# Kernel tuning notes

Hardware: AMD Instinct MI355X
Metric: run time of the kernel (lower is better)

The kernel has to match this reference:

```python
import jax, jax.numpy as jnp
import numpy as np

V, D, H, N, L = 400000, 300, 300, 346, 50


def _lstm_scan(x, Wih, Whh, b, reverse):
    # x: (L, N, din); torch gate order i, f, g, o
    Hh = Whh.shape[1]
    def step(carry, xt):
        h, c = carry
        g = xt @ Wih.T + h @ Whh.T + b
        i, f, gg, o = jnp.split(g, 4, axis=-1)
        c = jax.nn.sigmoid(f) * c + jax.nn.sigmoid(i) * jnp.tanh(gg)
        h = jax.nn.sigmoid(o) * jnp.tanh(c)
        return (h, c), h
    h0 = jnp.zeros((x.shape[1], Hh), x.dtype)
    (hT, _), outs = jax.lax.scan(step, (h0, h0), x, reverse=reverse)
    return hT, outs  # outs stacked in original time order


def _gate(h, W, U):
    # Faithful to torch gate_module: g_i broadcast over rows makes
    # g.repeat @ h_x == g_i * sum(h_x) and (1-g).repeat @ h_c_rep == (1-g_i)*m*h_c
    h_c = h[0]
    h_x = h[1:]
    m = h_x.shape[0]
    g = jax.nn.sigmoid(h_x @ W + h_c @ U)  # (m, 1)
    h_tuta = g * jnp.sum(h_x, axis=0) + (1.0 - g) * (m * h_c)
    return jnp.concatenate([h_c[None, :], h_tuta], axis=0)


def _gat(h, mask, W, a):
    # standard pyGAT GraphAttentionLayer (concat=True -> elu), alpha=0.01
    Wh = h @ W                              # (N, out)
    F = W.shape[1]
    e = jax.nn.leaky_relu((Wh @ a[:F]) + (Wh @ a[F:]).T, 0.01)  # (N, N)
    att = jax.nn.softmax(jnp.where(mask, e, -9e15), axis=1)
    return jax.nn.elu(att @ Wh)


def _forward(emb, Wih_l0f, Whh_l0f, b_l0f, Wih_l0b, Whh_l0b, b_l0b,
             Wih_l1f, Whh_l1f, b_l1f, Wih_l1b, Whh_l1b, b_l1b,
             W_gat, a_gat, gate_W, gate_U, FC1, FC2, Wlin, blin,
             tokens, adj):
    tok = tokens[0]                        # (N, L)
    x = jnp.swapaxes(emb[tok], 0, 1)       # (L, N, 300)
    hf0, of0 = _lstm_scan(x, Wih_l0f, Whh_l0f, b_l0f, False)
    hb0, ob0 = _lstm_scan(x, Wih_l0b, Whh_l0b, b_l0b, True)
    o0 = jnp.concatenate([of0, ob0], axis=-1)   # (L, N, 600)
    hf1, _ = _lstm_scan(o0, Wih_l1f, Whh_l1f, b_l1f, False)
    hb1, _ = _lstm_scan(o0, Wih_l1b, Whh_l1b, b_l1b, True)
    # h_n layout [l0f, l0b, l1f, l1b] -> per-node concat = 1200
    hs0 = jnp.concatenate([hf0, hb0, hf1, hb1], axis=-1)
    mask = adj > 0
    hs1 = _gat(jnp.concatenate([hs0, _gate(hs0, gate_W, gate_U)], axis=1), mask, W_gat, a_gat)
    hs2 = _gat(jnp.concatenate([hs1, _gate(hs1, gate_W, gate_U)], axis=1), mask, W_gat, a_gat)
    hc = jnp.broadcast_to(hs2[0], hs2.shape)          # repeat(346, 1)
    hc3 = jnp.tanh(jnp.concatenate([hc, hs2, hc * hs2, hc - hs2], axis=1) @ FC1)
    b_att = jnp.tanh(hc3 @ FC2)                       # (N, 1)
    ea = jnp.concatenate([jnp.mean(hs2, axis=0, keepdims=True), b_att.T @ hs2], axis=1)
    return jax.nn.softmax(ea @ Wlin.T + blin, axis=1)  # (1, 2)


def setup_inputs() -> dict:
    key = jax.random.key(0)
    ks = iter(jax.random.split(key, 40))
    def rn(shape, scale=0.05):
        return jax.random.normal(next(ks), shape, dtype=jnp.float32) * scale
    inp = {}
    inp["tokens"] = jax.random.randint(next(ks), (1, N, L), 0, V)
    inp["adj"] = jax.random.randint(next(ks), (N, N), 0, 2).astype(jnp.int32)
    inp["emb"] = rn((V, D), 1.0)
    for name, din in (("l0f", D), ("l0b", D), ("l1f", 2 * H), ("l1b", 2 * H)):
        inp[f"Wih_{name}"] = rn((4 * H, din))
        inp[f"Whh_{name}"] = rn((4 * H, H))
        inp[f"b_{name}"] = rn((4 * H,))
    inp["W_gat"] = rn((2400, 1200))
    inp["a_gat"] = rn((2400, 1))
    inp["gate_W"] = rn((1200, 1))
    inp["gate_U"] = rn((1200, 1))
    inp["FC1"] = rn((4800, 9600), 0.01)
    inp["FC2"] = rn((9600, 1), 0.01)
    inp["Wlin"] = rn((2, 2400))
    inp["blin"] = rn((2,))
    return inp


def reference(tokens, adj, emb, Wih_l0f, Whh_l0f, b_l0f, Wih_l0b, Whh_l0b, b_l0b,
              Wih_l1f, Whh_l1f, b_l1f, Wih_l1b, Whh_l1b, b_l1b,
              W_gat, a_gat, gate_W, gate_U, FC1, FC2, Wlin, blin):
    return _forward(emb, Wih_l0f, Whh_l0f, b_l0f, Wih_l0b, Whh_l0b, b_l0b,
                    Wih_l1f, Whh_l1f, b_l1f, Wih_l1b, Whh_l1b, b_l1b,
                    W_gat, a_gat, gate_W, gate_U, FC1, FC2, Wlin, blin,
                    tokens, adj)
```

## Files before the change

### kernel.cpp

```cpp
#include <hip/hip_runtime.h>
#include <hip/hip_bf16.h>
#include <math.h>

typedef __hip_bfloat16 bf16;
typedef __attribute__((ext_vector_type(8))) short bf16x8;
typedef __attribute__((ext_vector_type(4))) short bf16x4;
typedef __attribute__((ext_vector_type(4))) float f32x4;

constexpr int kN  = 346;
constexpr int kL  = 50;
constexpr int kD  = 300;
constexpr int kH  = 300;
constexpr int kG  = 1200;
constexpr int kNL = kN * kL;
constexpr int kNLp = 17408;
constexpr int kNp  = 384;
constexpr int kKp0 = 320;
constexpr int kKp1 = 608;
constexpr int kGp  = 1280;
constexpr int kHB  = 384;

__device__ inline float toF(float v) { return v; }
__device__ inline float toF(bf16 v) { return __bfloat162float(v); }
__device__ inline void storeC(float* p, float v) { *p = v; }
__device__ inline void storeC(bf16* p, float v) { *p = __float2bfloat16(v); }
__device__ inline float sigf(float x) { return 1.f / (1.f + expf(-x)); }
__device__ inline float bfbits2f(unsigned short u) {
    unsigned int x = ((unsigned int)u) << 16;
    float f; __builtin_memcpy(&f, &x, 4); return f;
}
__device__ inline short f2bf_bits(float f) {
    bf16 b = __float2bfloat16(f);
    short s; __builtin_memcpy(&s, &b, 2); return s;
}

template <int EPI, typename CT>
__global__ __launch_bounds__(256) void gemm_mfma(
    const bf16* __restrict__ A, const bf16* __restrict__ B, CT* __restrict__ C,
    int M, int N, int K, int lda, int ldb, int ldc,
    long sAz, long sBz, long sCz,
    const bf16* __restrict__ P, long sPz, const float* __restrict__ bias, long sbz)
{
    const short* Ag = (const short*)A + (size_t)blockIdx.z * sAz;
    const short* Bg = (const short*)B + (size_t)blockIdx.z * sBz;
    CT* Cg = C + (size_t)blockIdx.z * sCz;
    (void)P; (void)sPz; (void)bias; (void)sbz;

    __shared__ short As[128 * 40];
    __shared__ short Bs[128 * 40];
    int tid = threadIdx.x;
    int row0 = blockIdx.y * 128, col0 = blockIdx.x * 128;
    int wave = tid >> 6, lane = tid & 63;
    int wr = (wave >> 1) * 64, wc = (wave & 1) * 64;
    int lrow = lane & 15, lq = lane >> 4;

    f32x4 acc[4][4];
#pragma unroll
    for (int i = 0; i < 4; ++i)
#pragma unroll
        for (int j = 0; j < 4; ++j) acc[i][j] = (f32x4){0.f, 0.f, 0.f, 0.f};

    int sr = tid >> 2;
    int sc = (tid & 3) * 8;
    for (int k0 = 0; k0 < K; k0 += 32) {
        *(bf16x8*)&As[sr * 40 + sc]        = *(const bf16x8*)&Ag[(size_t)(row0 + sr) * lda + k0 + sc];
        *(bf16x8*)&As[(sr + 64) * 40 + sc] = *(const bf16x8*)&Ag[(size_t)(row0 + sr + 64) * lda + k0 + sc];
        *(bf16x8*)&Bs[sr * 40 + sc]        = *(const bf16x8*)&Bg[(size_t)(col0 + sr) * ldb + k0 + sc];
        *(bf16x8*)&Bs[(sr + 64) * 40 + sc] = *(const bf16x8*)&Bg[(size_t)(col0 + sr + 64) * ldb + k0 + sc];
        __syncthreads();
        bf16x8 aF[4], bF[4];
#pragma unroll
        for (int i = 0; i < 4; ++i) aF[i] = *(const bf16x8*)&As[(wr + i * 16 + lrow) * 40 + lq * 8];
#pragma unroll
        for (int j = 0; j < 4; ++j) bF[j] = *(const bf16x8*)&Bs[(wc + j * 16 + lrow) * 40 + lq * 8];
#pragma unroll
        for (int i = 0; i < 4; ++i)
#pragma unroll
            for (int j = 0; j < 4; ++j)
                acc[i][j] = __builtin_amdgcn_mfma_f32_16x16x32_bf16(aF[i], bF[j], acc[i][j], 0, 0, 0);
        __syncthreads();
    }
#pragma unroll
    for (int i = 0; i < 4; ++i) {
#pragma unroll
        for (int r = 0; r < 4; ++r) {
            int gm = row0 + wr + i * 16 + lq * 4 + r;
            if (gm >= M) continue;
#pragma unroll
            for (int j = 0; j < 4; ++j) {
                int gn = col0 + wc + j * 16 + lrow;
                if (gn >= N) continue;
                float v = acc[i][j][r];
                if constexpr (EPI == 3) v = v > 0.f ? v : (expf(v) - 1.f);
                if constexpr (EPI == 4) v = tanhf(v);
                storeC(&Cg[(size_t)gm * ldc + gn], v);
            }
        }
    }
}

__global__ void transpose_conv(const float* __restrict__ in, bf16* __restrict__ out,
                               int R, int Cc, int Rpad, int Cpad) {
    __shared__ float tile[32][33];
    int bc = blockIdx.x * 32, br = blockIdx.y * 32;
    int tx = threadIdx.x & 31, ty = threadIdx.x >> 5;
#pragma unroll
    for (int k = 0; k < 4; ++k) {
        int r = br + ty + 8 * k, c = bc + tx;
        tile[ty + 8 * k][tx] = (r < R && c < Cc) ? in[(size_t)r * Cc + c] : 0.f;
    }
    __syncthreads();
#pragma unroll
    for (int k = 0; k < 4; ++k) {
        int c = bc + ty + 8 * k, r = br + tx;
        if (c < Cpad && r < Rpad) out[(size_t)c * Rpad + r] = __float2bfloat16(tile[tx][ty + 8 * k]);
    }
}

__global__ void convert_pad_perm(const float* __restrict__ in, bf16* __restrict__ out,
                                 int Cc, int Cpad) {
    int idx = blockIdx.x * 256 + threadIdx.x;
    if (idx >= kGp * Cpad) return;
    int rp = idx / Cpad, c = idx - rp * Cpad;
    int j = rp >> 2, q = rp & 3;
    float v = (j < kH && c < Cc) ? in[(size_t)(q * kH + j) * Cc + c] : 0.f;
    out[idx] = __float2bfloat16(v);
}

__global__ void pack_biases_perm(const float* b0f, const float* b0b, const float* b1f,
                                 const float* b1b, float* b0, float* b1) {
    int i = blockIdx.x * 256 + threadIdx.x;
    if (i >= 2 * kGp) return;
    int dir = i / kGp, rp = i - dir * kGp;
    int j = rp >> 2, q = rp & 3;
    float v0 = 0.f, v1 = 0.f;
    if (j < kH) {
        v0 = dir ? b0b[q * kH + j] : b0f[q * kH + j];
        v1 = dir ? b1b[q * kH + j] : b1f[q * kH + j];
    }
    b0[i] = v0; b1[i] = v1;
}

__global__ void gather_kernel(const int* __restrict__ tokens, const float* __restrict__ emb,
                              bf16* __restrict__ x) {
    int idx = blockIdx.x * 256 + threadIdx.x;
    if (idx >= kNLp * kKp0) return;
    int row = idx / kKp0, d = idx - row * kKp0;
    float v = 0.f;
    if (row < kNL && d < kD) {
        int l = row / kN, n = row - l * kN;
        v = emb[(size_t)tokens[n * kL + l] * kD + d];
    }
    x[idx] = __float2bfloat16(v);
}

__device__ inline void group_barrier(int* bar, int target) {
    __syncthreads();
    if (threadIdx.x == 0) {
        __threadfence();
        __hip_atomic_fetch_add(bar, 1, __ATOMIC_RELAXED, __HIP_MEMORY_SCOPE_AGENT);
        while (__hip_atomic_load(bar, __ATOMIC_RELAXED, __HIP_MEMORY_SCOPE_AGENT) < target)
            __builtin_amdgcn_s_sleep(2);
    }
    __syncthreads();
    __threadfence();
}

template <bool WRITE_O0>
__global__ __launch_bounds__(256, 1) void lstm_scan_fused(
    const bf16* __restrict__ WhhP,
    const bf16* __restrict__ P,
    const float* __restrict__ biasP,
    bf16* __restrict__ hst,
    bf16* __restrict__ o0,
    int* __restrict__ bars)
{
    __shared__ short Bs[10][128][32];
    __shared__ float Gs[4 * 32 * 128];

    const int tid = threadIdx.x;
    const int bx  = blockIdx.x;
    const int cb  = bx % 10;
    const int rb  = (bx / 10) % 3;
    const int dir = bx / 30;
    int* bar = bars + dir * 3 + rb;

    const int wave = tid >> 6, lane = tid & 63;
    const int wr = (wave >> 1) * 64, wc = (wave & 1) * 64;
    const int lrow = lane & 15, lq = lane >> 4;
    const int col0 = cb * 128, row0 = rb * 128;

    {
        const short* Bg = (const short*)WhhP + (size_t)dir * kGp * kKp0;
        int sr = tid >> 2;
        int g  = tid & 3;
#pragma unroll
        for (int ch = 0; ch < 10; ++ch) {
            *(bf16x8*)&Bs[ch][sr][(g ^ ((sr >> 1) & 3)) * 8] =
                *(const bf16x8*)&Bg[(size_t)(col0 + sr) * kKp0 + ch * 32 + g * 8];
            *(bf16x8*)&Bs[ch][sr + 64][(g ^ (((sr + 64) >> 1) & 3)) * 8] =
                *(const bf16x8*)&Bg[(size_t)(col0 + sr + 64) * kKp0 + ch * 32 + g * 8];
        }
    }

    const int jj0 = (tid >> 5) * 4;
    const int pr0 = (tid & 31) * 4;
    const int jg0 = cb * 32 + jj0;
    const bool jok = jg0 < kH;

    float bias[4][4];
#pragma unroll
    for (int m = 0; m < 4; ++m) {
        f32x4 b4 = *(const f32x4*)&biasP[dir * kGp + col0 + (jj0 + m) * 4];
#pragma unroll
        for (int q = 0; q < 4; ++q) bias[m][q] = b4[q];
    }
    float cst[4][4];
#pragma unroll
    for (int m = 0; m < 4; ++m)
#pragma unroll
        for (int r = 0; r < 4; ++r) cst[m][r] = 0.f;

    short* o0s = (short*)o0;
    __syncthreads();

#pragma unroll 1
    for (int t = 0; t < kL; ++t) {
        const short* hr = (const short*)hst + ((size_t)(t & 1) * 2 + dir) * (kHB * kKp0);
        short* hw = (short*)hst + ((size_t)((t + 1) & 1) * 2 + dir) * (kHB * kKp0);
        const int teff = dir ? (kL - 1 - t) : t;
        const short* Pt = (const short*)P + (size_t)dir * kNL * kG + (size_t)teff * kN * kG;

        bf16x4 pv[4][4];
        if (jok) {
#pragma unroll
            for (int m = 0; m < 4; ++m)
#pragma unroll
                for (int rr = 0; rr < 4; ++rr) {
                    int rg = row0 + pr0 + rr;
                    if (rg < kN)
                        pv[m][rr] = *(const bf16x4*)&Pt[(size_t)rg * kG + (size_t)(jg0 + m) * 4];
                }
        }

        f32x4 acc[4][4];
#pragma unroll
        for (int i = 0; i < 4; ++i)
#pragma unroll
            for (int j = 0; j < 4; ++j) acc[i][j] = (f32x4){0.f, 0.f, 0.f, 0.f};

#pragma unroll
        for (int ch = 0; ch < 10; ++ch) {
            bf16x8 aF[4], bF[4];
#pragma unroll
            for (int i = 0; i < 4; ++i)
                aF[i] = *(const bf16x8*)&hr[(size_t)(row0 + wr + i * 16 + lrow) * kKp0 + ch * 32 + lq * 8];
#pragma unroll
            for (int j = 0; j < 4; ++j) {
                int brow = wc + j * 16 + lrow;
                bF[j] = *(const bf16x8*)&Bs[ch][brow][(lq ^ ((brow >> 1) & 3)) * 8];
            }
#pragma unroll
            for (int i = 0; i < 4; ++i)
#pragma unroll
                for (int j = 0; j < 4; ++j)
                    acc[i][j] = __builtin_amdgcn_mfma_f32_16x16x32_bf16(aF[i], bF[j], acc[i][j], 0, 0, 0);
        }

#pragma unroll
        for (int i = 0; i < 4; ++i) {
            int r0 = wr + i * 16 + lq * 4;
#pragma unroll
            for (int j = 0; j < 4; ++j) {
                int c = wc + j * 16 + lrow;
                int q = c & 3, jj = c >> 2;
                *(f32x4*)&Gs[(q * 32 + jj) * 128 + (r0 ^ ((jj & 7) << 2))] = acc[i][j];
            }
        }
        __syncthreads();

        if (jok) {
            float hval[4][4];
#pragma unroll
            for (int m = 0; m < 4; ++m) {
                int jjl = jj0 + m;
                int sw = (jjl & 7) << 2;
                f32x4 gi4 = *(const f32x4*)&Gs[(0 * 32 + jjl) * 128 + (pr0 ^ sw)];
                f32x4 gf4 = *(const f32x4*)&Gs[(1 * 32 + jjl) * 128 + (pr0 ^ sw)];
                f32x4 gg4 = *(const f32x4*)&Gs[(2 * 32 + jjl) * 128 + (pr0 ^ sw)];
                f32x4 go4 = *(const f32x4*)&Gs[(3 * 32 + jjl) * 128 + (pr0 ^ sw)];
#pragma unroll
                for (int rr = 0; rr < 4; ++rr) {
                    int rg = row0 + pr0 + rr;
                    if (rg >= kN) continue;
                    float iv = sigf(gi4[rr] + bfbits2f((unsigned short)pv[m][rr][0]) + bias[m][0]);
                    float fv = sigf(gf4[rr] + bfbits2f((unsigned short)pv[m][rr][1]) + bias[m][1]);
                    float gv = tanhf(gg4[rr] + bfbits2f((unsigned short)pv[m][rr][2]) + bias[m][2]);
                    float ov = sigf(go4[rr] + bfbits2f((unsigned short)pv[m][rr][3]) + bias[m][3]);
                    float cc = fv * cst[m][rr] + iv * gv;
                    cst[m][rr] = cc;
                    hval[rr][m] = ov * tanhf(cc);
                }
            }
#pragma unroll
            for (int rr = 0; rr < 4; ++rr) {
                int rg = row0 + pr0 + rr;
                if (rg >= kN) continue;
                bf16x4 hv;
#pragma unroll
                for (int m = 0; m < 4; ++m) hv[m] = f2bf_bits(hval[rr][m]);
                *(bf16x4*)&hw[(size_t)rg * kKp0 + jg0] = hv;
                if constexpr (WRITE_O0)
                    *(bf16x4*)&o0s[((size_t)teff * kN + rg) * kKp1 + dir * kH + jg0] = hv;
            }
        }

        group_barrier(bar, 10 * (t + 1));
    }
}

__global__ void concat_hs0(const bf16* __restrict__ hbf0, const bf16* __restrict__ hbf1,
                           float* __restrict__ hs0) {
    int idx = blockIdx.x * 256 + threadIdx.x;
    if (idx >= kN * kG) return;
    int r = idx / kG, c = idx - r * kG;
    float v;
    if (c < 300)       v = toF(hbf0[(size_t)r * kKp0 + c]);
    else if (c < 600)  v = toF(hbf0[(size_t)(kNp + r) * kKp0 + (c - 300)]);
    else if (c < 900)  v = toF(hbf1[(size_t)r * kKp0 + (c - 600)]);
    else               v = toF(hbf1[(size_t)(kNp + r) * kKp0 + (c - 900)]);
    hs0[idx] = v;
}

__global__ void colsum_kernel(const float* __restrict__ hs, float* __restrict__ sum_hx) {
    int c = blockIdx.x * 256 + threadIdx.x;
    if (c >= kG) return;
    float s = 0.f;
    for (int r = 1; r < kN; ++r) s += hs[(size_t)r * kG + c];
    sum_hx[c] = s;
}

__global__ void gate_rows(const float* __restrict__ hs, const float* __restrict__ gW,
                          const float* __restrict__ gU, const float* __restrict__ sum_hx,
                          bf16* __restrict__ hin) {
    __shared__ float red[256];
    int n = blockIdx.x, tid = threadIdx.x;
    for (int c = tid; c < kG; c += 256)
        hin[(size_t)n * 2400 + c] = __float2bfloat16(hs[(size_t)n * kG + c]);
    if (n == 0) {
        for (int c = tid; c < kG; c += 256)
            hin[1200 + c] = __float2bfloat16(hs[c]);
        return;
    }
    float dw = 0.f, du = 0.f;
    for (int c = tid; c < kG; c += 256) {
        dw += hs[(size_t)n * kG + c] * gW[c];
        du += hs[c] * gU[c];
    }
    red[tid] = dw; __syncthreads();
    for (int s = 128; s > 0; s >>= 1) { if (tid < s) red[tid] += red[tid + s]; __syncthreads(); }
    float sdw = red[0]; __syncthreads();
    red[tid] = du; __syncthreads();
    for (int s = 128; s > 0; s >>= 1) { if (tid < s) red[tid] += red[tid + s]; __syncthreads(); }
    float sdu = red[0]; __syncthreads();
    float gval = sigf(sdw + sdu);
    for (int c = tid; c < kG; c += 256) {
        float v = gval * sum_hx[c] + (1.f - gval) * (345.f * hs[c]);
        hin[(size_t)n * 2400 + 1200 + c] = __float2bfloat16(v);
    }
}

__global__ void gat_scores(const float* __restrict__ Wh, const float* __restrict__ a,
                           float* __restrict__ s1, float* __restrict__ s2) {
    __shared__ float red[256];
    int n = blockIdx.x, tid = threadIdx.x;
    float d1 = 0.f, d2 = 0.f;
    for (int c = tid; c < kG; c += 256) {
        float w = Wh[(size_t)n * kG + c];
        d1 += w * a[c];
        d2 += w * a[kG + c];
    }
    red[tid] = d1; __syncthreads();
    for (int s = 128; s > 0; s >>= 1) { if (tid < s) red[tid] += red[tid + s]; __syncthreads(); }
    if (tid == 0) s1[n] = red[0];
    __syncthreads();
    red[tid] = d2; __syncthreads();
    for (int s = 128; s > 0; s >>= 1) { if (tid < s) red[tid] += red[tid + s]; __syncthreads(); }
    if (tid == 0) s2[n] = red[0];
}

__global__ void gat_softmax(const float* __restrict__ s1, const float* __restrict__ s2,
                            const int* __restrict__ adj, bf16* __restrict__ att) {
    __shared__ float red[256];
    __shared__ float sh_m, sh_s;
    int i = blockIdx.x, tid = threadIdx.x;
    float s1i = s1[i];
    float m = -1e30f;
    for (int j = tid; j < kN; j += 256) {
        if (adj[i * kN + j] > 0) {
            float e = s1i + s2[j];
            e = e > 0.f ? e : 0.01f * e;
            m = fmaxf(m, e);
        }
    }
    red[tid] = m; __syncthreads();
    for (int s = 128; s > 0; s >>= 1) { if (tid < s) red[tid] = fmaxf(red[tid], red[tid + s]); __syncthreads(); }
    if (tid == 0) sh_m = red[0];
    __syncthreads();
    m = sh_m;
    float sum = 0.f;
    for (int j = tid; j < kN; j += 256) {
        if (adj[i * kN + j] > 0) {
            float e = s1i + s2[j];
            e = e > 0.f ? e : 0.01f * e;
            sum += expf(e - m);
        }
    }
    red[tid] = sum; __syncthreads();
    for (int s = 128; s > 0; s >>= 1) { if (tid < s) red[tid] += red[tid + s]; __syncthreads(); }
    if (tid == 0) sh_s = red[0];
    __syncthreads();
    float inv = sh_s > 0.f ? 1.f / sh_s : 0.f;
    for (int j = tid; j < kN; j += 256) {
        float v = 0.f;
        if (adj[i * kN + j] > 0) {
            float e = s1i + s2[j];
            e = e > 0.f ? e : 0.01f * e;
            v = expf(e - m) * inv;
        }
        att[(size_t)i * 352 + j] = __float2bfloat16(v);
    }
}

__global__ void build_cat4(const float* __restrict__ hs2, bf16* __restrict__ cat4) {
    int idx = blockIdx.x * 256 + threadIdx.x;
    if (idx >= kN * 4800) return;
    int r = idx / 4800, c = idx - r * 4800;
    int chunk = c / kG, cc = c - chunk * kG;
    float hc = hs2[cc];
    float hv = hs2[(size_t)r * kG + cc];
    float v = (chunk == 0) ? hc : (chunk == 1) ? hv : (chunk == 2) ? hc * hv : (hc - hv);
    cat4[idx] = __float2bfloat16(v);
}

__global__ void row_dot_tanh(const float* __restrict__ hc3, const float* __restrict__ FC2,
                             float* __restrict__ b_att) {
    __shared__ float red[256];
    int n = blockIdx.x, tid = threadIdx.x;
    float d = 0.f;
    for (int c = tid; c < 9600; c += 256) d += hc3[(size_t)n * 9600 + c] * FC2[c];
    red[tid] = d; __syncthreads();
    for (int s = 128; s > 0; s >>= 1) { if (tid < s) red[tid] += red[tid + s]; __syncthreads(); }
    if (tid == 0) b_att[n] = tanhf(red[0]);
}

__global__ void ea_kernel(const float* __restrict__ hs2, const float* __restrict__ b_att,
                          float* __restrict__ ea) {
    int c = blockIdx.x * 256 + threadIdx.x;
    if (c >= kG) return;
    float s = 0.f, w = 0.f;
    for (int r = 0; r < kN; ++r) {
        float v = hs2[(size_t)r * kG + c];
        s += v;
        w += b_att[r] * v;
    }
    ea[c] = s / (float)kN;
    ea[kG + c] = w;
}

__global__ void final_kernel(const float* __restrict__ ea, const float* __restrict__ Wlin,
                             const float* __restrict__ blin, float* __restrict__ out) {
    __shared__ float red[256];
    int tid = threadIdx.x;
    float l0 = 0.f, l1 = 0.f;
    for (int c = tid; c < 2400; c += 256) {
        float e = ea[c];
        l0 += e * Wlin[c];
        l1 += e * Wlin[2400 + c];
    }
    red[tid] = l0; __syncthreads();
    for (int s = 128; s > 0; s >>= 1) { if (tid < s) red[tid] += red[tid + s]; __syncthreads(); }
    l0 = red[0]; __syncthreads();
    red[tid] = l1; __syncthreads();
    for (int s = 128; s > 0; s >>= 1) { if (tid < s) red[tid] += red[tid + s]; __syncthreads(); }
    l1 = red[0];
    if (tid == 0) {
        l0 += blin[0];
        l1 += blin[1];
        float m = fmaxf(l0, l1);
        float e0 = expf(l0 - m), e1 = expf(l1 - m);
        float inv = 1.f / (e0 + e1);
        out[0] = e0 * inv;
        out[1] = e1 * inv;
    }
}

extern "C" void kernel_launch(void* const* d_in, const int* in_sizes, int n_in,
                              void* d_out, int out_size, void* d_ws, size_t ws_size,
                              hipStream_t stream) {
    const int*   tokens  = (const int*)d_in[0];
    const int*   adj     = (const int*)d_in[1];
    const float* emb     = (const float*)d_in[2];
    const float* Wih_l0f = (const float*)d_in[3];
    const float* Whh_l0f = (const float*)d_in[4];
    const float* b_l0f   = (const float*)d_in[5];
    const float* Wih_l0b = (const float*)d_in[6];
    const float* Whh_l0b = (const float*)d_in[7];
    const float* b_l0b   = (const float*)d_in[8];
    const float* Wih_l1f = (const float*)d_in[9];
    const float* Whh_l1f = (const float*)d_in[10];
    const float* b_l1f   = (const float*)d_in[11];
    const float* Wih_l1b = (const float*)d_in[12];
    const float* Whh_l1b = (const float*)d_in[13];
    const float* b_l1b   = (const float*)d_in[14];
    const float* W_gat   = (const float*)d_in[15];
    const float* a_gat   = (const float*)d_in[16];
    const float* gate_W  = (const float*)d_in[17];
    const float* gate_U  = (const float*)d_in[18];
    const float* FC1     = (const float*)d_in[19];
    const float* FC2     = (const float*)d_in[20];
    const float* Wlin    = (const float*)d_in[21];
    const float* blin    = (const float*)d_in[22];
    float* out = (float*)d_out;
    (void)in_sizes; (void)n_in; (void)out_size; (void)ws_size;

    char* base = (char*)d_ws;
    size_t off = 0;
    auto alloc = [&](size_t bytes) {
        size_t cur = off;
        off += (bytes + 255) & ~(size_t)255;
        return base + cur;
    };

    const size_t xPad_sz = (size_t)kNLp * kKp0 * 2;
    char* regA = alloc(94181120);
    bf16* xPad  = (bf16*)(regA);
    bf16* P0    = (bf16*)(regA + xPad_sz);
    bf16* P1    = (bf16*)(regA);
    bf16* WgatT = (bf16*)(regA);
    bf16* hin   = (bf16*)(regA + 6144000);
    bf16* att   = (bf16*)(regA + 7987200);
    bf16* FC1T  = (bf16*)(regA);
    const size_t gatScratch_sz = 8257536;

    char* o0r   = alloc((size_t)kNLp * kKp1 * 2);
    bf16*  o0   = (bf16*)o0r;
    float* hc3  = (float*)o0r;

    const size_t hst_sz = (size_t)2 * 2 * kHB * kKp0 * 2;
    char* hblk = alloc(hst_sz * 2 + 256);
    bf16* hstA = (bf16*)hblk;
    bf16* hstB = (bf16*)(hblk + hst_sz);
    int*  bars = (int*)(hblk + 2 * hst_sz);

    bf16* Wih0 = (bf16*)alloc((size_t)2 * kGp * kKp0 * 2);
    bf16* Wih1 = (bf16*)alloc((size_t)2 * kGp * kKp1 * 2);
    bf16* Whh0 = (bf16*)alloc((size_t)2 * kGp * kKp0 * 2);
    bf16* Whh1 = (bf16*)alloc((size_t)2 * kGp * kKp0 * 2);
    float* b0p = (float*)alloc(2 * kGp * 4);
    float* b1p = (float*)alloc(2 * kGp * 4);
    float* hsA = (float*)alloc((size_t)kN * kG * 4);
    float* hsB = (float*)alloc((size_t)kN * kG * 4);
    float* sum_hx = (float*)alloc(kG * 4);
    float* Wh  = (float*)alloc((size_t)kN * kG * 4);
    bf16*  WhT = (bf16*)alloc((size_t)kGp * 352 * 2);
    float* s1  = (float*)alloc(kN * 4);
    float* s2  = (float*)alloc(kN * 4);
    bf16*  cat4 = (bf16*)alloc((size_t)kNp * 4800 * 2);
    float* b_att = (float*)alloc(kN * 4);
    float* ea  = (float*)alloc(2400 * 4);

    hipMemsetAsync(hblk, 0, hst_sz * 2 + 256, stream);
    hipMemsetAsync(o0r, 0, (size_t)kNLp * kKp1 * 2, stream);
    hipMemsetAsync(cat4, 0, (size_t)kNp * 4800 * 2, stream);

    pack_biases_perm<<<10, 256, 0, stream>>>(b_l0f, b_l0b, b_l1f, b_l1b, b0p, b1p);
    int cpp0 = (kGp * kKp0 + 255) / 256;
    int cpp1 = (kGp * kKp1 + 255) / 256;
    convert_pad_perm<<<cpp0, 256, 0, stream>>>(Wih_l0f, Wih0,              kD,     kKp0);
    convert_pad_perm<<<cpp0, 256, 0, stream>>>(Wih_l0b, Wih0 + kGp * kKp0, kD,     kKp0);
    convert_pad_perm<<<cpp1, 256, 0, stream>>>(Wih_l1f, Wih1,              2 * kH, kKp1);
    convert_pad_perm<<<cpp1, 256, 0, stream>>>(Wih_l1b, Wih1 + kGp * kKp1, 2 * kH, kKp1);
    convert_pad_perm<<<cpp0, 256, 0, stream>>>(Whh_l0f, Whh0,              kH,     kKp0);
    convert_pad_perm<<<cpp0, 256, 0, stream>>>(Whh_l0b, Whh0 + kGp * kKp0, kH,     kKp0);
    convert_pad_perm<<<cpp0, 256, 0, stream>>>(Whh_l1f, Whh1,              kH,     kKp0);
    convert_pad_perm<<<cpp0, 256, 0, stream>>>(Whh_l1b, Whh1 + kGp * kKp0, kH,     kKp0);

    gather_kernel<<<(kNLp * kKp0 + 255) / 256, 256, 0, stream>>>(tokens, emb, xPad);

    gemm_mfma<0, bf16><<<dim3(10, kNLp / 128, 2), 256, 0, stream>>>(
        xPad, Wih0, P0, kNL, kG, kKp0, kKp0, kKp0, kG,
        0, (long)kGp * kKp0, (long)kNL * kG, nullptr, 0, nullptr, 0);

    lstm_scan_fused<true><<<60, 256, 0, stream>>>(Whh0, P0, b0p, hstA, o0, bars);

    gemm_mfma<0, bf16><<<dim3(10, kNLp / 128, 2), 256, 0, stream>>>(
        o0, Wih1, P1, kNL, kG, kKp1, kKp1, kKp1, kG,
        0, (long)kGp * kKp1, (long)kNL * kG, nullptr, 0, nullptr, 0);

    lstm_scan_fused<false><<<60, 256, 0, stream>>>(Whh1, P1, b1p, hstB, nullptr, bars + 6);

    concat_hs0<<<(kN * kG + 255) / 256, 256, 0, stream>>>(hstA, hstB, hsA);

    hipMemsetAsync(regA, 0, gatScratch_sz, stream);
    transpose_conv<<<dim3(kGp / 32, 2400 / 32), 256, 0, stream>>>(W_gat, WgatT, 2400, kG, 2400, kGp);

    float* hsIn = hsA;
    float* hsOut = hsB;
    for (int it = 0; it < 2; ++it) {
        colsum_kernel<<<(kG + 255) / 256, 256, 0, stream>>>(hsIn, sum_hx);
        gate_rows<<<kN, 256, 0, stream>>>(hsIn, gate_W, gate_U, sum_hx, hin);
        gemm_mfma<0, float><<<dim3(10, 3, 1), 256, 0, stream>>>(
            hin, WgatT, Wh, kN, kG, 2400, 2400, 2400, kG,
            0, 0, 0, nullptr, 0, nullptr, 0);
        gat_scores<<<kN, 256, 0, stream>>>(Wh, a_gat, s1, s2);
        gat_softmax<<<kN, 256, 0, stream>>>(s1, s2, adj, att);
        transpose_conv<<<dim3(kGp / 32, 352 / 32), 256, 0, stream>>>(Wh, WhT, kN, kG, 352, kGp);
        gemm_mfma<3, float><<<dim3(10, 3, 1), 256, 0, stream>>>(
            att, WhT, hsOut, kN, kG, 352, 352, 352, kG,
            0, 0, 0, nullptr, 0, nullptr, 0);
        float* tmp = hsIn; hsIn = hsOut; hsOut = tmp;
    }

    build_cat4<<<(kN * 4800 + 255) / 256, 256, 0, stream>>>(hsIn, cat4);
    transpose_conv<<<dim3(9600 / 32, 4800 / 32), 256, 0, stream>>>(FC1, FC1T, 4800, 9600, 4800, 9600);
    gemm_mfma<4, float><<<dim3(75, 3, 1), 256, 0, stream>>>(
        cat4, FC1T, hc3, kN, 9600, 4800, 4800, 4800, 9600,
        0, 0, 0, nullptr, 0, nullptr, 0);
    row_dot_tanh<<<kN, 256, 0, stream>>>(hc3, FC2, b_att);
    ea_kernel<<<(kG + 255) / 256, 256, 0, stream>>>(hsIn, b_att, ea);
    final_kernel<<<1, 256, 0, stream>>>(ea, Wlin, blin, out);
}
```

Baseline: 3.709 ms.

## Drop threadfences in LSTM group barrier using agent-scope atomic h loads/stores

Removes the two __threadfence calls from the inter-block group barrier. Coherence of the recurrent hidden-state exchange now relies on relaxed agent-scope 64-bit atomic stores and loads plus an explicit vmcnt(0) wait before the barrier. It also prefetches the next timestep's precomputed input-gate slice before the barrier so that load latency overlaps the spin-wait. The cost removed is the cache-flush and invalidate overhead paid on each of the 50 recurrent steps. In exchange, the A-fragment loads are split into two 8-byte atomic loads, and correctness now depends on relaxed ordering being enough.

New measurement: 3.651 ms. Within noise of the previous version (-1.6%).

```diff
diff --git a/kernel.cpp b/kernel.cpp
--- a/kernel.cpp
+++ b/kernel.cpp
@@ -34,6 +34,13 @@
     short s; __builtin_memcpy(&s, &b, 2); return s;
 }
 
+__device__ inline void g_store8(short* p, unsigned long long v) {
+    __hip_atomic_store((unsigned long long*)p, v, __ATOMIC_RELAXED, __HIP_MEMORY_SCOPE_AGENT);
+}
+__device__ inline unsigned long long g_load8(const short* p) {
+    return __hip_atomic_load((const unsigned long long*)p, __ATOMIC_RELAXED, __HIP_MEMORY_SCOPE_AGENT);
+}
+
 template <int EPI, typename CT>
 __global__ __launch_bounds__(256) void gemm_mfma(
     const bf16* __restrict__ A, const bf16* __restrict__ B, CT* __restrict__ C,
@@ -155,15 +162,14 @@
 }
 
 __device__ inline void group_barrier(int* bar, int target) {
+    asm volatile("s_waitcnt vmcnt(0)" ::: "memory");
     __syncthreads();
     if (threadIdx.x == 0) {
-        __threadfence();
         __hip_atomic_fetch_add(bar, 1, __ATOMIC_RELAXED, __HIP_MEMORY_SCOPE_AGENT);
         while (__hip_atomic_load(bar, __ATOMIC_RELAXED, __HIP_MEMORY_SCOPE_AGENT) < target)
             __builtin_amdgcn_s_sleep(2);
     }
     __syncthreads();
-    __threadfence();
 }
 
 template <bool WRITE_O0>
@@ -222,6 +228,23 @@
         for (int r = 0; r < 4; ++r) cst[m][r] = 0.f;
 
     short* o0s = (short*)o0;
+
+    bf16x4 pv[4][4];
+    auto prefetchP = [&](int t) {
+        const int teff = dir ? (kL - 1 - t) : t;
+        const short* Pt = (const short*)P + (size_t)dir * kNL * kG + (size_t)teff * kN * kG;
+        if (jok) {
+#pragma unroll
+            for (int m = 0; m < 4; ++m)
+#pragma unroll
+                for (int rr = 0; rr < 4; ++rr) {
+                    int rg = row0 + pr0 + rr;
+                    if (rg < kN)
+                        pv[m][rr] = *(const bf16x4*)&Pt[(size_t)rg * kG + (size_t)(jg0 + m) * 4];
+                }
+        }
+    };
+    prefetchP(0);
     __syncthreads();
 
 #pragma unroll 1
@@ -229,19 +252,6 @@
         const short* hr = (const short*)hst + ((size_t)(t & 1) * 2 + dir) * (kHB * kKp0);
         short* hw = (short*)hst + ((size_t)((t + 1) & 1) * 2 + dir) * (kHB * kKp0);
         const int teff = dir ? (kL - 1 - t) : t;
-        const short* Pt = (const short*)P + (size_t)dir * kNL * kG + (size_t)teff * kN * kG;
-
-        bf16x4 pv[4][4];
-        if (jok) {
-#pragma unroll
-            for (int m = 0; m < 4; ++m)
-#pragma unroll
-                for (int rr = 0; rr < 4; ++rr) {
-                    int rg = row0 + pr0 + rr;
-                    if (rg < kN)
-                        pv[m][rr] = *(const bf16x4*)&Pt[(size_t)rg * kG + (size_t)(jg0 + m) * 4];
-                }
-        }
 
         f32x4 acc[4][4];
 #pragma unroll
@@ -253,8 +263,13 @@
         for (int ch = 0; ch < 10; ++ch) {
             bf16x8 aF[4], bF[4];
 #pragma unroll
-            for (int i = 0; i < 4; ++i)
-                aF[i] = *(const bf16x8*)&hr[(size_t)(row0 + wr + i * 16 + lrow) * kKp0 + ch * 32 + lq * 8];
+            for (int i = 0; i < 4; ++i) {
+                const short* ap = &hr[(size_t)(row0 + wr + i * 16 + lrow) * kKp0 + ch * 32 + lq * 8];
+                union { unsigned long long u[2]; bf16x8 v; } cv;
+                cv.u[0] = g_load8(ap);
+                cv.u[1] = g_load8(ap + 4);
+                aF[i] = cv.v;
+            }
 #pragma unroll
             for (int j = 0; j < 4; ++j) {
                 int brow = wc + j * 16 + lrow;
@@ -306,14 +321,16 @@
             for (int rr = 0; rr < 4; ++rr) {
                 int rg = row0 + pr0 + rr;
                 if (rg >= kN) continue;
-                bf16x4 hv;
-#pragma unroll
-                for (int m = 0; m < 4; ++m) hv[m] = f2bf_bits(hval[rr][m]);
-                *(bf16x4*)&hw[(size_t)rg * kKp0 + jg0] = hv;
+                union { bf16x4 v; unsigned long long u; } hv;
+#pragma unroll
+                for (int m = 0; m < 4; ++m) hv.v[m] = f2bf_bits(hval[rr][m]);
+                g_store8(&hw[(size_t)rg * kKp0 + jg0], hv.u);
                 if constexpr (WRITE_O0)
-                    *(bf16x4*)&o0s[((size_t)teff * kN + rg) * kKp1 + dir * kH + jg0] = hv;
+                    *(bf16x4*)&o0s[((size_t)teff * kN + rg) * kKp1 + dir * kH + jg0] = hv.v;
             }
         }
+
+        if (t + 1 < kL) prefetchP(t + 1);
 
         group_barrier(bar, 10 * (t + 1));
     }
```
